# Kernel optimization log

Measured on AMD Instinct MI355X. Metric: run time of the kernel, lower is better.

The kernel has to match this reference:

```python
import jax, jax.numpy as jnp
import numpy as np

N = 50000
E = 600000
IN_C = 128
HID_C = 128
OUT_C = 128


def _glorot(key, shape):
    fan_in, fan_out = shape[0], shape[1]
    lim = np.sqrt(6.0 / (fan_in + fan_out))
    return jax.random.uniform(key, shape, jnp.float32, -lim, lim)


def setup_inputs() -> dict:
    key = jax.random.key(0)
    ks = jax.random.split(key, 10)
    x = jax.random.normal(ks[0], (N, IN_C), jnp.float32)
    edge_index = jax.random.randint(ks[1], (2, E), 0, N, jnp.int64)
    return {
        "x": x,
        "edge_index": edge_index,
        # SAGEConv1: lin_l (aggregated, with bias) and lin_r (root, no bias)
        "W1_l": _glorot(ks[2], (IN_C, HID_C)),
        "b1_l": jnp.zeros((HID_C,), jnp.float32),
        "W1_r": _glorot(ks[3], (IN_C, HID_C)),
        # SAGEConv2
        "W2_l": _glorot(ks[4], (HID_C, OUT_C)),
        "b2_l": jnp.zeros((OUT_C,), jnp.float32),
        "W2_r": _glorot(ks[5], (HID_C, OUT_C)),
        # final Linear(hidden+out -> out)
        "W_lin": _glorot(ks[6], (HID_C + OUT_C, OUT_C)),
        "b_lin": jnp.zeros((OUT_C,), jnp.float32),
    }


def _sage_conv(x, src, dst, W_l, b_l, W_r):
    # mean-aggregate source features onto destination nodes
    msg = x[src]                                   # [E, C] gather
    agg = jax.ops.segment_sum(msg, dst, num_segments=N)        # [N, C]
    cnt = jax.ops.segment_sum(jnp.ones((src.shape[0],), x.dtype), dst,
                              num_segments=N)                   # [N]
    mean = agg / jnp.maximum(cnt, 1.0)[:, None]
    return mean @ W_l + b_l + x @ W_r


def reference(x, edge_index, W1_l, b1_l, W1_r, W2_l, b2_l, W2_r, W_lin, b_lin):
    src, dst = edge_index[0], edge_index[1]
    x1 = jax.nn.relu(_sage_conv(x, src, dst, W1_l, b1_l, W1_r))   # [N, HID]
    x2 = jax.nn.relu(_sage_conv(x1, src, dst, W2_l, b2_l, W2_r))  # [N, OUT]
    return jnp.concatenate([x1, x2], axis=-1) @ W_lin + b_lin     # [N, OUT]
```

## Files before the change

### kernel.cpp

```cpp
#include <hip/hip_runtime.h>


typedef _Float16 f16;
typedef __attribute__((ext_vector_type(2))) _Float16 f16x2;
typedef __attribute__((ext_vector_type(4))) _Float16 f16x4;
typedef __attribute__((ext_vector_type(8))) _Float16 f16x8;
typedef __attribute__((ext_vector_type(4))) float f32x4;

__global__ void prep_kernel(const float* __restrict__ x, f16* __restrict__ xh, int n4,
                            const int* __restrict__ ei, int* __restrict__ deg, int E,
                            const float* __restrict__ W1l, const float* __restrict__ W1r,
                            const float* __restrict__ W2l, const float* __restrict__ W2r,
                            const float* __restrict__ Wlin, f16* __restrict__ wt,
                            int cb, int db) {
  int b = blockIdx.x;
  if (b < cb) {
    int i = b * 256 + threadIdx.x;
    if (i < n4) {
      const float4 v = ((const float4*)x)[i];
      f16x4 h = { (f16)v.x, (f16)v.y, (f16)v.z, (f16)v.w };
      ((f16x4*)xh)[i] = h;
    }
  } else if (b < cb + db) {
    int e = (b - cb) * 256 + threadIdx.x;
    if (e < E) atomicAdd(&deg[ei[E + e]], 1);
  } else {
    int tid = (b - cb - db) * 256 + threadIdx.x;
    int w = tid >> 15, idx = tid & 32767;
    int j = idx & 7, n = (idx >> 3) & 127, chunk = idx >> 10;
    int k = chunk * 8 + j;
    float v;
    if (w == 0) v = (k < 128) ? W1l[k * 128 + n] : W1r[(k - 128) * 128 + n];
    else if (w == 1) v = (k < 128) ? W2l[k * 128 + n] : W2r[(k - 128) * 128 + n];
    else v = Wlin[k * 128 + n];
    wt[tid] = (f16)v;
  }
}

__global__ void scan_block_kernel(const int* __restrict__ in, int* __restrict__ out,
                                  int* __restrict__ sums, int n) {
  __shared__ int s[2][1024];
  int t = threadIdx.x;
  int gid = blockIdx.x * 1024 + t;
  int v = (gid < n) ? in[gid] : 0;
  int cur = 0;
  s[0][t] = v;
  __syncthreads();
  for (int ofs = 1; ofs < 1024; ofs <<= 1) {
    int nv = s[cur][t] + ((t >= ofs) ? s[cur][t - ofs] : 0);
    s[cur ^ 1][t] = nv;
    cur ^= 1;
    __syncthreads();
  }
  if (gid < n) out[gid] = s[cur][t] - v;
  if (t == 1023) sums[blockIdx.x] = s[cur][1023];
}

__global__ void scan_add_kernel(int* __restrict__ off, const int* __restrict__ sums,
                                int* __restrict__ cur, int n, int E) {
  __shared__ int prefix_s;
  int b = blockIdx.x;
  if (threadIdx.x < 64) {
    int v = ((int)threadIdx.x < b) ? sums[threadIdx.x] : 0;
#pragma unroll
    for (int ofs = 1; ofs < 64; ofs <<= 1) v += __shfl_xor(v, ofs);
    if (threadIdx.x == 0) prefix_s = v;
  }
  __syncthreads();
  int gid = b * 1024 + threadIdx.x;
  if (gid < n) { off[gid] += prefix_s; cur[gid] = 0; }
  if (gid == 0) off[n] = E;
}

__global__ void fill_kernel(const int* __restrict__ ei, const int* __restrict__ off,
                            int* __restrict__ cursor, int* __restrict__ srcs, int E) {
  int e = blockIdx.x * blockDim.x + threadIdx.x;
  if (e < E) {
    int src = ei[e], dst = ei[E + e];
    int pos = atomicAdd(&cursor[dst], 1);
    srcs[off[dst] + pos] = src;
  }
}

#define AGG_R 6
__global__ void aggregate_kernel(const f16* __restrict__ feat, const int* __restrict__ off,
                                 const int* __restrict__ srcs, f16* __restrict__ meanf, int n) {
  int pair = (int)((blockIdx.x * blockDim.x + threadIdx.x) >> 6);
  int w0 = pair * 2;
  if (w0 >= n) return;
  int w1 = w0 + 1;
  int lane = threadIdx.x & 63;
  int sub = lane >> 4, n15 = lane & 15;
  int beg0 = off[w0], end0 = off[w0 + 1];
  int beg1 = end0;
  int end1 = (w1 < n) ? off[w1 + 1] : end0;
  int deg0 = end0 - beg0, deg1 = end1 - beg1;

  int s0[AGG_R], s1[AGG_R];
  bool v0[AGG_R], v1[AGG_R];
#pragma unroll
  for (int k = 0; k < AGG_R; ++k) {
    int p = 4 * k + sub;
    v0[k] = p < deg0;  s0[k] = v0[k] ? srcs[beg0 + p] : 0;
    v1[k] = p < deg1;  s1[k] = v1[k] ? srcs[beg1 + p] : 0;
  }
  f16x8 g0[AGG_R], g1[AGG_R];
#pragma unroll
  for (int k = 0; k < AGG_R; ++k) {
    if (v0[k]) g0[k] = *(const f16x8*)(feat + (size_t)s0[k] * 128 + n15 * 8);
    if (v1[k]) g1[k] = *(const f16x8*)(feat + (size_t)s1[k] * 128 + n15 * 8);
  }
  float acc0[8] = {}, acc1[8] = {};
#pragma unroll
  for (int k = 0; k < AGG_R; ++k) {
    if (v0[k]) {
#pragma unroll
      for (int j = 0; j < 8; ++j) acc0[j] += (float)g0[k][j];
    }
    if (v1[k]) {
#pragma unroll
      for (int j = 0; j < 8; ++j) acc1[j] += (float)g1[k][j];
    }
  }
  for (int e = beg0 + 4 * AGG_R; e < end0; e += 4) {
    if (sub < end0 - e) {
      int s = srcs[e + sub];
      f16x8 g = *(const f16x8*)(feat + (size_t)s * 128 + n15 * 8);
#pragma unroll
      for (int j = 0; j < 8; ++j) acc0[j] += (float)g[j];
    }
  }
  for (int e = beg1 + 4 * AGG_R; e < end1; e += 4) {
    if (sub < end1 - e) {
      int s = srcs[e + sub];
      f16x8 g = *(const f16x8*)(feat + (size_t)s * 128 + n15 * 8);
#pragma unroll
      for (int j = 0; j < 8; ++j) acc1[j] += (float)g[j];
    }
  }
#pragma unroll
  for (int j = 0; j < 8; ++j) {
    acc0[j] += __shfl_xor(acc0[j], 16);
    acc0[j] += __shfl_xor(acc0[j], 32);
    acc1[j] += __shfl_xor(acc1[j], 16);
    acc1[j] += __shfl_xor(acc1[j], 32);
  }
  if (sub == 0) {
    float inv = 1.0f / fmaxf((float)deg0, 1.0f);
    f16x8 o;
#pragma unroll
    for (int j = 0; j < 8; ++j) o[j] = (f16)(acc0[j] * inv);
    *(f16x8*)(meanf + (size_t)w0 * 128 + n15 * 8) = o;
  } else if (sub == 1 && w1 < n) {
    float inv = 1.0f / fmaxf((float)deg1, 1.0f);
    f16x8 o;
#pragma unroll
    for (int j = 0; j < 8; ++j) o[j] = (f16)(acc1[j] * inv);
    *(f16x8*)(meanf + (size_t)w1 * 128 + n15 * 8) = o;
  }
}

template <bool RELU, bool OUT16>
__global__ __launch_bounds__(256, 2) void gemm_kernel(
    const f16* __restrict__ U, const f16* __restrict__ V, const f16* __restrict__ Wt,
    const float* __restrict__ bias, void* __restrict__ outp, int M) {
  __shared__ f16 ldsb[32768];
  int tid = threadIdx.x;
  int wave = tid >> 6, lane = tid & 63;
  int quad = lane >> 4, n15 = lane & 15;
  int m0 = blockIdx.x * 128 + wave * 32;
  int kq = quad * 8;

  f16x8 a[2][8];
#pragma unroll
  for (int r = 0; r < 2; ++r) {
    int row = m0 + r * 16 + n15;
    int rowc = row < M ? row : M - 1;
    const f16* bu = U + (size_t)rowc * 128 + kq;
    const f16* bv = V + (size_t)rowc * 128 + kq;
#pragma unroll
    for (int kk = 0; kk < 4; ++kk) a[r][kk] = *(const f16x8*)(bu + kk * 32);
#pragma unroll
    for (int kk = 4; kk < 8; ++kk) a[r][kk] = *(const f16x8*)(bv + (kk - 4) * 32);
  }

#pragma unroll
  for (int it = 0; it < 16; ++it) {
    int idx = it * 256 + tid;
    ((f16x8*)ldsb)[idx] = ((const f16x8*)Wt)[idx];
  }
  __syncthreads();

  f32x4 acc[2][8] = {};
#pragma unroll
  for (int kk = 0; kk < 8; ++kk) {
#pragma unroll
    for (int t = 0; t < 8; ++t) {
      f16x8 b = ((const f16x8*)ldsb)[(kk * 4 + quad) * 128 + t * 16 + n15];
#pragma unroll
      for (int r = 0; r < 2; ++r)
        acc[r][t] = __builtin_amdgcn_mfma_f32_16x16x32_f16(a[r][kk], b, acc[r][t], 0, 0, 0);
    }
  }

  int rbase0 = m0 + quad * 4;
#pragma unroll
  for (int t = 0; t < 8; ++t) {
    float bv = bias[t * 16 + n15];
#pragma unroll
    for (int r = 0; r < 2; ++r) {
#pragma unroll
      for (int i = 0; i < 4; ++i) {
        int row = rbase0 + r * 16 + i;
        if (row < M) {
          float v = acc[r][t][i] + bv;
          if (RELU) v = fmaxf(v, 0.f);
          size_t idx = (size_t)row * 128 + t * 16 + n15;
          if (OUT16) ((f16*)outp)[idx] = (f16)v;
          else       ((float*)outp)[idx] = v;
        }
      }
    }
  }
}

extern "C" void kernel_launch(void* const* d_in, const int* in_sizes, int n_in,
                              void* d_out, int out_size, void* d_ws, size_t ws_size,
                              hipStream_t stream) {
  (void)n_in; (void)out_size; (void)ws_size;
  const float* x    = (const float*)d_in[0];
  const int*   ei   = (const int*)d_in[1];
  const float* W1l  = (const float*)d_in[2];
  const float* b1l  = (const float*)d_in[3];
  const float* W1r  = (const float*)d_in[4];
  const float* W2l  = (const float*)d_in[5];
  const float* b2l  = (const float*)d_in[6];
  const float* W2r  = (const float*)d_in[7];
  const float* Wlin = (const float*)d_in[8];
  const float* blin = (const float*)d_in[9];
  const int N = in_sizes[0] / 128;
  const int E = in_sizes[1] / 2;

  char* ws = (char*)d_ws;
  size_t o = 0;
  auto alloc = [&](size_t bytes) {
    char* p = ws + o;
    o = (o + bytes + 255) & ~(size_t)255;
    return p;
  };
  f16* xh   = (f16*)alloc((size_t)N * 128 * 2);
  f16* x1h  = (f16*)alloc((size_t)N * 128 * 2);
  f16* x2h  = (f16*)alloc((size_t)N * 128 * 2);
  f16* mh   = (f16*)alloc((size_t)N * 128 * 2);
  f16* wt   = (f16*)alloc((size_t)3 * 32768 * 2);
  int* deg  = (int*)alloc((size_t)N * 4);
  int* cur  = (int*)alloc((size_t)N * 4);
  int* off  = (int*)alloc(((size_t)N + 1) * 4);
  int* srcs = (int*)alloc((size_t)E * 4);
  int* sums = (int*)alloc(64 * 4);
  f16* wt1 = wt, *wt2 = wt + 32768, *wt3 = wt + 65536;

  hipMemsetAsync(deg, 0, (size_t)N * 4, stream);

  const int n4 = N * 128 / 4;
  const int cb = (n4 + 255) / 256;
  const int db = (E + 255) / 256;
  const int wb = (3 * 32768) / 256;
  prep_kernel<<<cb + db + wb, 256, 0, stream>>>(x, xh, n4, ei, deg, E,
                                                W1l, W1r, W2l, W2r, Wlin, wt, cb, db);

  const int nb = (N + 1023) / 1024;
  scan_block_kernel<<<nb, 1024, 0, stream>>>(deg, off, sums, N);
  scan_add_kernel<<<nb, 1024, 0, stream>>>(off, sums, cur, N, E);
  fill_kernel<<<db, 256, 0, stream>>>(ei, off, cur, srcs, E);

  const int aggBlocks  = ((N + 1) / 2 + 3) / 4;
  const int gemmBlocks = (N + 127) / 128;

  aggregate_kernel<<<aggBlocks, 256, 0, stream>>>(xh, off, srcs, mh, N);
  gemm_kernel<true, true><<<gemmBlocks, 256, 0, stream>>>(mh, xh, wt1, b1l, x1h, N);
  aggregate_kernel<<<aggBlocks, 256, 0, stream>>>(x1h, off, srcs, mh, N);
  gemm_kernel<true, true><<<gemmBlocks, 256, 0, stream>>>(mh, x1h, wt2, b2l, x2h, N);
  gemm_kernel<false, false><<<gemmBlocks, 256, 0, stream>>>(x1h, x2h, wt3, blin, d_out, N);
}
```

Measured before the change: 260.6 us.

## Fuse neighbor mean aggregation with SAGE layer GEMM into one kernel

Replaces the separate aggregate and GEMM kernels for each SAGE layer with one kernel. Each lane gathers and averages neighbor rows for one node directly into MFMA A-fragment registers, then multiplies by LDS-resident weights, adds bias and applies ReLU. This removes the intermediate mean buffer write and read and two launches per layer. The gather mapping changes from four lanes sharing a node's edges to one node per lane with the loop bounded by the wave's max degree, so degree imbalance can cause divergence, and each 64-row block reloads the full 64KB weight tile.

```diff
diff --git a/kernel.cpp b/kernel.cpp
--- a/kernel.cpp
+++ b/kernel.cpp
@@ -2,7 +2,6 @@
 
 
 typedef _Float16 f16;
-typedef __attribute__((ext_vector_type(2))) _Float16 f16x2;
 typedef __attribute__((ext_vector_type(4))) _Float16 f16x4;
 typedef __attribute__((ext_vector_type(8))) _Float16 f16x8;
 typedef __attribute__((ext_vector_type(4))) float f32x4;
@@ -82,81 +81,115 @@
   }
 }
 
-#define AGG_R 6
-__global__ void aggregate_kernel(const f16* __restrict__ feat, const int* __restrict__ off,
-                                 const int* __restrict__ srcs, f16* __restrict__ meanf, int n) {
-  int pair = (int)((blockIdx.x * blockDim.x + threadIdx.x) >> 6);
-  int w0 = pair * 2;
-  if (w0 >= n) return;
-  int w1 = w0 + 1;
-  int lane = threadIdx.x & 63;
-  int sub = lane >> 4, n15 = lane & 15;
-  int beg0 = off[w0], end0 = off[w0 + 1];
-  int beg1 = end0;
-  int end1 = (w1 < n) ? off[w1 + 1] : end0;
-  int deg0 = end0 - beg0, deg1 = end1 - beg1;
-
-  int s0[AGG_R], s1[AGG_R];
-  bool v0[AGG_R], v1[AGG_R];
-#pragma unroll
-  for (int k = 0; k < AGG_R; ++k) {
-    int p = 4 * k + sub;
-    v0[k] = p < deg0;  s0[k] = v0[k] ? srcs[beg0 + p] : 0;
-    v1[k] = p < deg1;  s1[k] = v1[k] ? srcs[beg1 + p] : 0;
-  }
-  f16x8 g0[AGG_R], g1[AGG_R];
-#pragma unroll
-  for (int k = 0; k < AGG_R; ++k) {
-    if (v0[k]) g0[k] = *(const f16x8*)(feat + (size_t)s0[k] * 128 + n15 * 8);
-    if (v1[k]) g1[k] = *(const f16x8*)(feat + (size_t)s1[k] * 128 + n15 * 8);
-  }
-  float acc0[8] = {}, acc1[8] = {};
-#pragma unroll
-  for (int k = 0; k < AGG_R; ++k) {
-    if (v0[k]) {
-#pragma unroll
-      for (int j = 0; j < 8; ++j) acc0[j] += (float)g0[k][j];
-    }
-    if (v1[k]) {
-#pragma unroll
-      for (int j = 0; j < 8; ++j) acc1[j] += (float)g1[k][j];
-    }
-  }
-  for (int e = beg0 + 4 * AGG_R; e < end0; e += 4) {
-    if (sub < end0 - e) {
-      int s = srcs[e + sub];
-      f16x8 g = *(const f16x8*)(feat + (size_t)s * 128 + n15 * 8);
-#pragma unroll
-      for (int j = 0; j < 8; ++j) acc0[j] += (float)g[j];
-    }
-  }
-  for (int e = beg1 + 4 * AGG_R; e < end1; e += 4) {
-    if (sub < end1 - e) {
-      int s = srcs[e + sub];
-      f16x8 g = *(const f16x8*)(feat + (size_t)s * 128 + n15 * 8);
-#pragma unroll
-      for (int j = 0; j < 8; ++j) acc1[j] += (float)g[j];
-    }
-  }
-#pragma unroll
-  for (int j = 0; j < 8; ++j) {
-    acc0[j] += __shfl_xor(acc0[j], 16);
-    acc0[j] += __shfl_xor(acc0[j], 32);
-    acc1[j] += __shfl_xor(acc1[j], 16);
-    acc1[j] += __shfl_xor(acc1[j], 32);
-  }
-  if (sub == 0) {
-    float inv = 1.0f / fmaxf((float)deg0, 1.0f);
-    f16x8 o;
-#pragma unroll
-    for (int j = 0; j < 8; ++j) o[j] = (f16)(acc0[j] * inv);
-    *(f16x8*)(meanf + (size_t)w0 * 128 + n15 * 8) = o;
-  } else if (sub == 1 && w1 < n) {
-    float inv = 1.0f / fmaxf((float)deg1, 1.0f);
-    f16x8 o;
-#pragma unroll
-    for (int j = 0; j < 8; ++j) o[j] = (f16)(acc1[j] * inv);
-    *(f16x8*)(meanf + (size_t)w1 * 128 + n15 * 8) = o;
+__global__ __launch_bounds__(256, 2) void sage_layer_kernel(
+    const f16* __restrict__ feat, const int* __restrict__ off,
+    const int* __restrict__ srcs, const f16* __restrict__ Wt,
+    const float* __restrict__ bias, f16* __restrict__ outp, int M) {
+  __shared__ f16 ldsw[32768];
+  int tid = threadIdx.x;
+  int w = tid >> 6, lane = tid & 63;
+  int quad = lane >> 4, n15 = lane & 15;
+  int base = blockIdx.x * 64;
+  int node = base + w * 16 + n15;
+
+  int gi0 = node < M ? node : M;
+  int gi1 = node + 1 < M ? node + 1 : M;
+  int begL = off[gi0], endL = off[gi1];
+  int degL = endL - begL;
+  int maxd = degL;
+#pragma unroll
+  for (int ofs = 1; ofs < 64; ofs <<= 1) {
+    int o = __shfl_xor(maxd, ofs);
+    maxd = o > maxd ? o : maxd;
+  }
+
+  float acc[4][8] = {};
+  const f16* fq = feat + quad * 8;
+  int r = 0;
+  for (; r + 2 <= maxd; r += 2) {
+    bool a0 = r < degL, a1 = r + 1 < degL;
+    int s0 = a0 ? srcs[begL + r] : 0;
+    int s1 = a1 ? srcs[begL + r + 1] : 0;
+    const f16* p0 = fq + (size_t)s0 * 128;
+    const f16* p1 = fq + (size_t)s1 * 128;
+    f16x8 g0[4], g1[4];
+    if (a0) {
+#pragma unroll
+      for (int kk = 0; kk < 4; ++kk) g0[kk] = *(const f16x8*)(p0 + kk * 32);
+    }
+    if (a1) {
+#pragma unroll
+      for (int kk = 0; kk < 4; ++kk) g1[kk] = *(const f16x8*)(p1 + kk * 32);
+    }
+    if (a0) {
+#pragma unroll
+      for (int kk = 0; kk < 4; ++kk)
+#pragma unroll
+        for (int j = 0; j < 8; ++j) acc[kk][j] += (float)g0[kk][j];
+    }
+    if (a1) {
+#pragma unroll
+      for (int kk = 0; kk < 4; ++kk)
+#pragma unroll
+        for (int j = 0; j < 8; ++j) acc[kk][j] += (float)g1[kk][j];
+    }
+  }
+  if (r < maxd && r < degL) {
+    int s0 = srcs[begL + r];
+    const f16* p0 = fq + (size_t)s0 * 128;
+#pragma unroll
+    for (int kk = 0; kk < 4; ++kk) {
+      f16x8 g = *(const f16x8*)(p0 + kk * 32);
+#pragma unroll
+      for (int j = 0; j < 8; ++j) acc[kk][j] += (float)g[j];
+    }
+  }
+
+  float inv = 1.0f / fmaxf((float)degL, 1.0f);
+  f16x8 am[4];
+#pragma unroll
+  for (int kk = 0; kk < 4; ++kk)
+#pragma unroll
+    for (int j = 0; j < 8; ++j) am[kk][j] = (f16)(acc[kk][j] * inv);
+
+  int rowc = node < M ? node : M - 1;
+  f16x8 ag[4];
+  {
+    const f16* ps = feat + (size_t)rowc * 128 + quad * 8;
+#pragma unroll
+    for (int j = 0; j < 4; ++j) ag[j] = *(const f16x8*)(ps + j * 32);
+  }
+
+#pragma unroll
+  for (int it = 0; it < 16; ++it) {
+    int idx = it * 256 + tid;
+    ((f16x8*)ldsw)[idx] = ((const f16x8*)Wt)[idx];
+  }
+  __syncthreads();
+
+  f32x4 accd[8] = {};
+#pragma unroll
+  for (int kk = 0; kk < 8; ++kk) {
+    f16x8 a = (kk < 4) ? am[kk] : ag[kk - 4];
+#pragma unroll
+    for (int t = 0; t < 8; ++t) {
+      f16x8 b = ((const f16x8*)ldsw)[(kk * 4 + quad) * 128 + t * 16 + n15];
+      accd[t] = __builtin_amdgcn_mfma_f32_16x16x32_f16(a, b, accd[t], 0, 0, 0);
+    }
+  }
+
+  int rbase = base + w * 16 + quad * 4;
+#pragma unroll
+  for (int t = 0; t < 8; ++t) {
+    float bv = bias[t * 16 + n15];
+#pragma unroll
+    for (int i = 0; i < 4; ++i) {
+      int row = rbase + i;
+      if (row < M) {
+        float v = fmaxf(accd[t][i] + bv, 0.f);
+        outp[(size_t)row * 128 + t * 16 + n15] = (f16)v;
+      }
+    }
   }
 }
 
@@ -251,7 +284,6 @@
   f16* xh   = (f16*)alloc((size_t)N * 128 * 2);
   f16* x1h  = (f16*)alloc((size_t)N * 128 * 2);
   f16* x2h  = (f16*)alloc((size_t)N * 128 * 2);
-  f16* mh   = (f16*)alloc((size_t)N * 128 * 2);
   f16* wt   = (f16*)alloc((size_t)3 * 32768 * 2);
   int* deg  = (int*)alloc((size_t)N * 4);
   int* cur  = (int*)alloc((size_t)N * 4);
@@ -274,12 +306,10 @@
   scan_add_kernel<<<nb, 1024, 0, stream>>>(off, sums, cur, N, E);
   fill_kernel<<<db, 256, 0, stream>>>(ei, off, cur, srcs, E);
 
-  const int aggBlocks  = ((N + 1) / 2 + 3) / 4;
-  const int gemmBlocks = (N + 127) / 128;
-
-  aggregate_kernel<<<aggBlocks, 256, 0, stream>>>(xh, off, srcs, mh, N);
-  gemm_kernel<true, true><<<gemmBlocks, 256, 0, stream>>>(mh, xh, wt1, b1l, x1h, N);
-  aggregate_kernel<<<aggBlocks, 256, 0, stream>>>(x1h, off, srcs, mh, N);
-  gemm_kernel<true, true><<<gemmBlocks, 256, 0, stream>>>(mh, x1h, wt2, b2l, x2h, N);
+  const int layerBlocks = (N + 63) / 64;
+  const int gemmBlocks  = (N + 127) / 128;
+
+  sage_layer_kernel<<<layerBlocks, 256, 0, stream>>>(xh,  off, srcs, wt1, b1l, x1h, N);
+  sage_layer_kernel<<<layerBlocks, 256, 0, stream>>>(x1h, off, srcs, wt2, b2l, x2h, N);
   gemm_kernel<false, false><<<gemmBlocks, 256, 0, stream>>>(x1h, x2h, wt3, blin, d_out, N);
 }
```

Result: slower. 275.5 us (+5.7%).
